# Performance work log

Hardware: AMD Instinct MI355X
Metric: run time of the kernel (lower is better)

The kernel has to match this reference:

```python
import jax, jax.numpy as jnp
import numpy as np


def setup_inputs() -> dict:
    key = jax.random.key(0)
    k1, k2 = jax.random.split(key)
    B, D, NUM_CLASSES = 8192, 128, 100
    features = jax.random.normal(k1, (B, D), dtype=jnp.float32)
    labels = jax.random.randint(k2, (B,), 0, NUM_CLASSES, dtype=jnp.int64)
    return {"features": features, "labels": labels}


def reference(features, labels):
    # temperature=0.07, clamp(min=0.01) -> 0.07
    TEMP = 0.07
    B = features.shape[0]
    dt = features.dtype

    # positive mask from labels: [B, B]
    mask = (labels[:, None] == labels[None, :]).astype(dt)

    # L2 normalize rows (F.normalize: x / max(||x||, eps))
    norm = jnp.sqrt(jnp.sum(features * features, axis=1, keepdims=True))
    f = features / jnp.maximum(norm, 1e-8)

    # similarity matrix, scaled and clamped to [-10, 10]
    sim = jnp.clip(jnp.matmul(f, f.T) / TEMP, -10.0, 10.0)

    eye = jnp.eye(B, dtype=dt)
    exp_sim = jnp.exp(sim)

    pos_sum = jnp.maximum(jnp.sum(exp_sim * (mask - eye), axis=1), 1e-8)
    neg_sum = jnp.maximum(jnp.sum(exp_sim * (1.0 - eye), axis=1), 1e-8)

    loss = -jnp.log(pos_sum / neg_sum)
    # NaN guard as in the original (returns 0 if any NaN)
    return jnp.where(jnp.any(jnp.isnan(loss)), jnp.zeros((), dt), jnp.mean(loss))
```

## Files before the change

### kernel.cpp

```cpp
#include <hip/hip_runtime.h>
#include <hip/hip_bf16.h>


using short8  = __attribute__((ext_vector_type(8))) short;
using floatx4 = __attribute__((ext_vector_type(4))) float;

constexpr int   Bn = 8192;
constexpr int   Dk = 128;
constexpr int   NSLICE = 32;
constexpr float PRESCALE = 4.5398160f;
constexpr float CLAMP    = 14.4269504f;
constexpr float LN2      = 0.69314718056f;

__global__ __launch_bounds__(256) void normalize_k(
    const float* __restrict__ feat, unsigned short* __restrict__ fb,
    float* __restrict__ out) {
  if (blockIdx.x == 0 && threadIdx.x == 0) *out = 0.f;
  const int row  = blockIdx.x * 4 + (threadIdx.x >> 6);
  const int lane = threadIdx.x & 63;
  const float2 v = ((const float2*)(feat + (size_t)row * Dk))[lane];
  float s = v.x * v.x + v.y * v.y;
#pragma unroll
  for (int m = 1; m < 64; m <<= 1) s += __shfl_xor(s, m);
  const float inv = PRESCALE / fmaxf(sqrtf(s), 1e-8f);
  __hip_bfloat16 b0 = __float2bfloat16(v.x * inv);
  __hip_bfloat16 b1 = __float2bfloat16(v.y * inv);
  ushort2 o;
  o.x = __builtin_bit_cast(unsigned short, b0);
  o.y = __builtin_bit_cast(unsigned short, b1);
  ((ushort2*)(fb + (size_t)row * Dk))[lane] = o;
}

__global__ __launch_bounds__(256, 2) void simloss_k(
    const unsigned short* __restrict__ fb, const int* __restrict__ labels,
    float* __restrict__ rowpos2, float* __restrict__ rowneg2) {
  __shared__ __align__(16) short Bsh[256 * Dk];

  const int t     = threadIdx.x;
  const int lane  = t & 63;
  const int wave  = t >> 6;
  const int quad  = lane >> 4;
  const int lr    = lane & 15;
  const int jbase = blockIdx.x * 256;

  {
    const int chunk = t & 15;
    const int r0    = t >> 4;
#pragma unroll
    for (int it = 0; it < 16; ++it) {
      const int row = r0 + it * 16;
      const short8 v = *(const short8*)((const short*)fb +
                          (size_t)(jbase + row) * Dk + chunk * 8);
      *(short8*)(Bsh + row * Dk + ((chunk ^ (row & 7)) * 8)) = v;
    }
  }

  int labj16[8];
#pragma unroll
  for (int j = 0; j < 8; ++j) {
    const int l0 = labels[jbase + (2 * j) * 16 + lr];
    const int l1 = labels[jbase + (2 * j + 1) * 16 + lr];
    labj16[j] = l0 | (l1 << 16);
  }

  bool dl[4];
#pragma unroll
  for (int r = 0; r < 4; ++r) dl[r] = (quad * 4 + r) == lr;

  const int sw = lr & 7;
  const int c0 = ((0 + quad) ^ sw) * 8;
  const int c1 = ((4 + quad) ^ sw) * 8;
  const int c2 = ((8 + quad) ^ sw) * 8;
  const int c3 = ((12 + quad) ^ sw) * 8;

  __syncthreads();

#pragma unroll 1
  for (int p = 0; p < 2; ++p) {
    const int ibase = blockIdx.y * 256 + wave * 64 + p * 32;

    short8 A[2][4];
#pragma unroll
    for (int tt = 0; tt < 2; ++tt) {
      const short* ap = (const short*)fb + (size_t)(ibase + tt * 16 + lr) * Dk + quad * 8;
#pragma unroll
      for (int kk = 0; kk < 4; ++kk) A[tt][kk] = *(const short8*)(ap + kk * 32);
    }

    int li[2][4];
#pragma unroll
    for (int tt = 0; tt < 2; ++tt)
#pragma unroll
      for (int r = 0; r < 4; ++r)
        li[tt][r] = labels[ibase + tt * 16 + quad * 4 + r];

    float pos[2][4] = {};
    float neg[2][4] = {};

#pragma unroll
    for (int jt = 0; jt < 16; ++jt) {
      const short* bp = Bsh + (jt * 16 + lr) * Dk;
      const short8 B0 = *(const short8*)(bp + c0);
      const short8 B1 = *(const short8*)(bp + c1);
      const short8 B2 = *(const short8*)(bp + c2);
      const short8 B3 = *(const short8*)(bp + c3);

      floatx4 acc0 = {0.f, 0.f, 0.f, 0.f};
      floatx4 acc1 = {0.f, 0.f, 0.f, 0.f};
      acc0 = __builtin_amdgcn_mfma_f32_16x16x32_bf16(A[0][0], B0, acc0, 0, 0, 0);
      acc1 = __builtin_amdgcn_mfma_f32_16x16x32_bf16(A[1][0], B0, acc1, 0, 0, 0);
      acc0 = __builtin_amdgcn_mfma_f32_16x16x32_bf16(A[0][1], B1, acc0, 0, 0, 0);
      acc1 = __builtin_amdgcn_mfma_f32_16x16x32_bf16(A[1][1], B1, acc1, 0, 0, 0);
      acc0 = __builtin_amdgcn_mfma_f32_16x16x32_bf16(A[0][2], B2, acc0, 0, 0, 0);
      acc1 = __builtin_amdgcn_mfma_f32_16x16x32_bf16(A[1][2], B2, acc1, 0, 0, 0);
      acc0 = __builtin_amdgcn_mfma_f32_16x16x32_bf16(A[0][3], B3, acc0, 0, 0, 0);
      acc1 = __builtin_amdgcn_mfma_f32_16x16x32_bf16(A[1][3], B3, acc1, 0, 0, 0);

      const int j0 = jbase + jt * 16;
      const int lj = (jt & 1) ? (labj16[jt >> 1] >> 16) : (labj16[jt >> 1] & 0xffff);
      float e0, e1, e2, e3;
      e0 = __builtin_amdgcn_exp2f(__builtin_amdgcn_fmed3f(acc0[0], -CLAMP, CLAMP));
      e1 = __builtin_amdgcn_exp2f(__builtin_amdgcn_fmed3f(acc0[1], -CLAMP, CLAMP));
      e2 = __builtin_amdgcn_exp2f(__builtin_amdgcn_fmed3f(acc0[2], -CLAMP, CLAMP));
      e3 = __builtin_amdgcn_exp2f(__builtin_amdgcn_fmed3f(acc0[3], -CLAMP, CLAMP));
      if (j0 == ibase) {
        if (dl[0]) e0 = 0.f;
        if (dl[1]) e1 = 0.f;
        if (dl[2]) e2 = 0.f;
        if (dl[3]) e3 = 0.f;
      }
      neg[0][0] += e0; neg[0][1] += e1; neg[0][2] += e2; neg[0][3] += e3;
      pos[0][0] += (li[0][0] == lj) ? e0 : 0.f;
      pos[0][1] += (li[0][1] == lj) ? e1 : 0.f;
      pos[0][2] += (li[0][2] == lj) ? e2 : 0.f;
      pos[0][3] += (li[0][3] == lj) ? e3 : 0.f;
      e0 = __builtin_amdgcn_exp2f(__builtin_amdgcn_fmed3f(acc1[0], -CLAMP, CLAMP));
      e1 = __builtin_amdgcn_exp2f(__builtin_amdgcn_fmed3f(acc1[1], -CLAMP, CLAMP));
      e2 = __builtin_amdgcn_exp2f(__builtin_amdgcn_fmed3f(acc1[2], -CLAMP, CLAMP));
      e3 = __builtin_amdgcn_exp2f(__builtin_amdgcn_fmed3f(acc1[3], -CLAMP, CLAMP));
      if (j0 == ibase + 16) {
        if (dl[0]) e0 = 0.f;
        if (dl[1]) e1 = 0.f;
        if (dl[2]) e2 = 0.f;
        if (dl[3]) e3 = 0.f;
      }
      neg[1][0] += e0; neg[1][1] += e1; neg[1][2] += e2; neg[1][3] += e3;
      pos[1][0] += (li[1][0] == lj) ? e0 : 0.f;
      pos[1][1] += (li[1][1] == lj) ? e1 : 0.f;
      pos[1][2] += (li[1][2] == lj) ? e2 : 0.f;
      pos[1][3] += (li[1][3] == lj) ? e3 : 0.f;
    }

#pragma unroll
    for (int tt = 0; tt < 2; ++tt)
#pragma unroll
      for (int r = 0; r < 4; ++r) {
        float p2 = pos[tt][r], n2 = neg[tt][r];
#pragma unroll
        for (int m = 1; m < 16; m <<= 1) {
          p2 += __shfl_xor(p2, m);
          n2 += __shfl_xor(n2, m);
        }
        if (lr == 0) {
          const int row = ibase + tt * 16 + quad * 4 + r;
          rowpos2[(size_t)blockIdx.x * Bn + row] = p2;
          rowneg2[(size_t)blockIdx.x * Bn + row] = n2;
        }
      }

    __builtin_amdgcn_sched_barrier(0);
  }
}

__global__ __launch_bounds__(256) void finalize_k(
    const float* __restrict__ rowpos2, const float* __restrict__ rowneg2,
    float* __restrict__ out) {
  const int row = blockIdx.x * 256 + threadIdx.x;
  float p = 0.f, n = 0.f;
#pragma unroll
  for (int s = 0; s < NSLICE; ++s) {
    p += rowpos2[(size_t)s * Bn + row];
    n += rowneg2[(size_t)s * Bn + row];
  }
  p = fmaxf(p, 1e-8f);
  n = fmaxf(n, 1e-8f);
  float loss = LN2 * (__builtin_amdgcn_logf(n) - __builtin_amdgcn_logf(p));
#pragma unroll
  for (int m = 1; m < 64; m <<= 1) loss += __shfl_xor(loss, m);
  __shared__ float partial[4];
  const int lane = threadIdx.x & 63, w = threadIdx.x >> 6;
  if (lane == 0) partial[w] = loss;
  __syncthreads();
  if (threadIdx.x == 0) {
    const float s = partial[0] + partial[1] + partial[2] + partial[3];
    atomicAdd(out, s * (1.0f / (float)Bn));
  }
}

extern "C" void kernel_launch(void* const* d_in, const int* in_sizes, int n_in,
                              void* d_out, int out_size, void* d_ws, size_t ws_size,
                              hipStream_t stream) {
  const float* feat   = (const float*)d_in[0];
  const int*   labels = (const int*)d_in[1];
  float* out = (float*)d_out;

  unsigned short* fb = (unsigned short*)d_ws;
  float* rowpos2 = (float*)((char*)d_ws + (size_t)Bn * Dk * sizeof(unsigned short));
  float* rowneg2 = rowpos2 + (size_t)NSLICE * Bn;

  normalize_k<<<Bn / 4, 256, 0, stream>>>(feat, fb, out);
  dim3 grid(NSLICE, 32);
  simloss_k<<<grid, 256, 0, stream>>>(fb, labels, rowpos2, rowneg2);
  finalize_k<<<Bn / 256, 256, 0, stream>>>(rowpos2, rowneg2, out);
}
```

Before: 110.6 us.

## Switch similarity GEMM from bf16 to fp8 MFMA with permuted layout

```diff
diff --git a/kernel.cpp b/kernel.cpp
--- a/kernel.cpp
+++ b/kernel.cpp
@@ -2,8 +2,8 @@
 #include <hip/hip_bf16.h>
 
 
-using short8  = __attribute__((ext_vector_type(8))) short;
 using floatx4 = __attribute__((ext_vector_type(4))) float;
+using llong2  = __attribute__((ext_vector_type(2))) long long;
 
 constexpr int   Bn = 8192;
 constexpr int   Dk = 128;
@@ -13,7 +13,7 @@
 constexpr float LN2      = 0.69314718056f;
 
 __global__ __launch_bounds__(256) void normalize_k(
-    const float* __restrict__ feat, unsigned short* __restrict__ fb,
+    const float* __restrict__ feat, unsigned char* __restrict__ fb,
     float* __restrict__ out) {
   if (blockIdx.x == 0 && threadIdx.x == 0) *out = 0.f;
   const int row  = blockIdx.x * 4 + (threadIdx.x >> 6);
@@ -23,18 +23,16 @@
 #pragma unroll
   for (int m = 1; m < 64; m <<= 1) s += __shfl_xor(s, m);
   const float inv = PRESCALE / fmaxf(sqrtf(s), 1e-8f);
-  __hip_bfloat16 b0 = __float2bfloat16(v.x * inv);
-  __hip_bfloat16 b1 = __float2bfloat16(v.y * inv);
-  ushort2 o;
-  o.x = __builtin_bit_cast(unsigned short, b0);
-  o.y = __builtin_bit_cast(unsigned short, b1);
-  ((ushort2*)(fb + (size_t)row * Dk))[lane] = o;
+  const int packed = __builtin_amdgcn_cvt_pk_fp8_f32(v.x * inv, v.y * inv, 0, false);
+  const int k0 = 2 * lane;
+  const int p  = ((k0 & 31) >> 3) * 32 + (k0 >> 5) * 8 + (k0 & 7);
+  *(unsigned short*)(fb + (size_t)row * Dk + p) = (unsigned short)(packed & 0xffff);
 }
 
 __global__ __launch_bounds__(256, 2) void simloss_k(
-    const unsigned short* __restrict__ fb, const int* __restrict__ labels,
+    const unsigned char* __restrict__ fb, const int* __restrict__ labels,
     float* __restrict__ rowpos2, float* __restrict__ rowneg2) {
-  __shared__ __align__(16) short Bsh[256 * Dk];
+  __shared__ __align__(16) unsigned char Bsh[256 * Dk];
 
   const int t     = threadIdx.x;
   const int lane  = t & 63;
@@ -44,14 +42,13 @@
   const int jbase = blockIdx.x * 256;
 
   {
-    const int chunk = t & 15;
-    const int r0    = t >> 4;
-#pragma unroll
-    for (int it = 0; it < 16; ++it) {
-      const int row = r0 + it * 16;
-      const short8 v = *(const short8*)((const short*)fb +
-                          (size_t)(jbase + row) * Dk + chunk * 8);
-      *(short8*)(Bsh + row * Dk + ((chunk ^ (row & 7)) * 8)) = v;
+    const int chunk = t & 7;
+    const int r0    = t >> 3;
+#pragma unroll
+    for (int it = 0; it < 8; ++it) {
+      const int row = r0 + it * 32;
+      const llong2 v = *(const llong2*)(fb + (size_t)(jbase + row) * Dk + chunk * 16);
+      *(llong2*)(Bsh + row * Dk + ((chunk ^ (row & 7)) * 16)) = v;
     }
   }
 
@@ -67,11 +64,9 @@
 #pragma unroll
   for (int r = 0; r < 4; ++r) dl[r] = (quad * 4 + r) == lr;
 
-  const int sw = lr & 7;
-  const int c0 = ((0 + quad) ^ sw) * 8;
-  const int c1 = ((4 + quad) ^ sw) * 8;
-  const int c2 = ((8 + quad) ^ sw) * 8;
-  const int c3 = ((12 + quad) ^ sw) * 8;
+  const int sw  = lr & 7;
+  const int ch0 = ((quad * 2)     ^ sw) * 16;
+  const int ch1 = ((quad * 2 + 1) ^ sw) * 16;
 
   __syncthreads();
 
@@ -79,12 +74,14 @@
   for (int p = 0; p < 2; ++p) {
     const int ibase = blockIdx.y * 256 + wave * 64 + p * 32;
 
-    short8 A[2][4];
-#pragma unroll
-    for (int tt = 0; tt < 2; ++tt) {
-      const short* ap = (const short*)fb + (size_t)(ibase + tt * 16 + lr) * Dk + quad * 8;
-#pragma unroll
-      for (int kk = 0; kk < 4; ++kk) A[tt][kk] = *(const short8*)(ap + kk * 32);
+    llong2 A0lo, A0hi, A1lo, A1hi;
+    {
+      const unsigned char* ap0 = fb + (size_t)(ibase + lr) * Dk + quad * 32;
+      const unsigned char* ap1 = ap0 + 16 * Dk;
+      A0lo = *(const llong2*)(ap0);
+      A0hi = *(const llong2*)(ap0 + 16);
+      A1lo = *(const llong2*)(ap1);
+      A1hi = *(const llong2*)(ap1 + 16);
     }
 
     int li[2][4];
@@ -99,22 +96,20 @@
 
 #pragma unroll
     for (int jt = 0; jt < 16; ++jt) {
-      const short* bp = Bsh + (jt * 16 + lr) * Dk;
-      const short8 B0 = *(const short8*)(bp + c0);
-      const short8 B1 = *(const short8*)(bp + c1);
-      const short8 B2 = *(const short8*)(bp + c2);
-      const short8 B3 = *(const short8*)(bp + c3);
+      const unsigned char* bp = Bsh + (jt * 16 + lr) * Dk;
+      const llong2 Blo = *(const llong2*)(bp + ch0);
+      const llong2 Bhi = *(const llong2*)(bp + ch1);
 
       floatx4 acc0 = {0.f, 0.f, 0.f, 0.f};
       floatx4 acc1 = {0.f, 0.f, 0.f, 0.f};
-      acc0 = __builtin_amdgcn_mfma_f32_16x16x32_bf16(A[0][0], B0, acc0, 0, 0, 0);
-      acc1 = __builtin_amdgcn_mfma_f32_16x16x32_bf16(A[1][0], B0, acc1, 0, 0, 0);
-      acc0 = __builtin_amdgcn_mfma_f32_16x16x32_bf16(A[0][1], B1, acc0, 0, 0, 0);
-      acc1 = __builtin_amdgcn_mfma_f32_16x16x32_bf16(A[1][1], B1, acc1, 0, 0, 0);
-      acc0 = __builtin_amdgcn_mfma_f32_16x16x32_bf16(A[0][2], B2, acc0, 0, 0, 0);
-      acc1 = __builtin_amdgcn_mfma_f32_16x16x32_bf16(A[1][2], B2, acc1, 0, 0, 0);
-      acc0 = __builtin_amdgcn_mfma_f32_16x16x32_bf16(A[0][3], B3, acc0, 0, 0, 0);
-      acc1 = __builtin_amdgcn_mfma_f32_16x16x32_bf16(A[1][3], B3, acc1, 0, 0, 0);
+      acc0 = __builtin_amdgcn_mfma_f32_16x16x32_fp8_fp8(A0lo.x, Blo.x, acc0, 0, 0, 0);
+      acc1 = __builtin_amdgcn_mfma_f32_16x16x32_fp8_fp8(A1lo.x, Blo.x, acc1, 0, 0, 0);
+      acc0 = __builtin_amdgcn_mfma_f32_16x16x32_fp8_fp8(A0lo.y, Blo.y, acc0, 0, 0, 0);
+      acc1 = __builtin_amdgcn_mfma_f32_16x16x32_fp8_fp8(A1lo.y, Blo.y, acc1, 0, 0, 0);
+      acc0 = __builtin_amdgcn_mfma_f32_16x16x32_fp8_fp8(A0hi.x, Bhi.x, acc0, 0, 0, 0);
+      acc1 = __builtin_amdgcn_mfma_f32_16x16x32_fp8_fp8(A1hi.x, Bhi.x, acc1, 0, 0, 0);
+      acc0 = __builtin_amdgcn_mfma_f32_16x16x32_fp8_fp8(A0hi.y, Bhi.y, acc0, 0, 0, 0);
+      acc1 = __builtin_amdgcn_mfma_f32_16x16x32_fp8_fp8(A1hi.y, Bhi.y, acc1, 0, 0, 0);
 
       const int j0 = jbase + jt * 16;
       const int lj = (jt & 1) ? (labj16[jt >> 1] >> 16) : (labj16[jt >> 1] & 0xffff);
@@ -204,8 +199,8 @@
   const int*   labels = (const int*)d_in[1];
   float* out = (float*)d_out;
 
-  unsigned short* fb = (unsigned short*)d_ws;
-  float* rowpos2 = (float*)((char*)d_ws + (size_t)Bn * Dk * sizeof(unsigned short));
+  unsigned char* fb = (unsigned char*)d_ws;
+  float* rowpos2 = (float*)((char*)d_ws + (size_t)Bn * Dk);
   float* rowneg2 = rowpos2 + (size_t)NSLICE * Bn;
 
   normalize_k<<<Bn / 4, 256, 0, stream>>>(feat, fb, out);
```

Result: faster. 102.5 us (-7.3%).
